# Performance work log

Hardware: AMD Instinct MI355X
Metric: run time of the kernel (lower is better)

The kernel has to match this reference:

```python
import jax, jax.numpy as jnp
import numpy as np

H1, H2, H3 = 32, 64, 64
NODEN = 12
NODES_PER_GRAPH = NODEN + 2  # 14
N = 700000                   # 50000 graphs * 14 nodes
E = 4000000


def setup_inputs() -> dict:
    key = jax.random.key(0)
    ks = jax.random.split(key, 8)
    x = jax.random.normal(ks[0], (N, H1), dtype=jnp.float32)
    edges = jax.random.randint(ks[1], (2, E), 0, N, dtype=jnp.int64)
    W1 = jax.random.normal(ks[2], (H1, H2), dtype=jnp.float32) / np.sqrt(H1).astype(np.float32)
    b1 = jnp.zeros((H2,), jnp.float32)
    W2 = jax.random.normal(ks[3], (H2, H3), dtype=jnp.float32) / np.sqrt(H2).astype(np.float32)
    b2 = jnp.zeros((H3,), jnp.float32)
    Wfc = jax.random.normal(ks[4], (H3 * NODES_PER_GRAPH, 1), dtype=jnp.float32) / np.sqrt(H3 * NODES_PER_GRAPH).astype(np.float32)
    bfc = jnp.zeros((1,), jnp.float32)
    return {"x": x, "edges": edges, "W1": W1, "b1": b1, "W2": W2, "b2": b2, "Wfc": Wfc, "bfc": bfc}


def gcn_conv(x, src, dst, W, b, n):
    # PyG GCNConv: h = X W; add self-loops; norm = deg^-1/2[src]*deg^-1/2[dst]
    h = x @ W  # [N, out]
    ones = jnp.ones(src.shape[0], dtype=h.dtype)
    deg = jax.ops.segment_sum(ones, dst, num_segments=n) + jnp.asarray(1.0, h.dtype)  # +1 self-loop
    dinv = jax.lax.rsqrt(deg)  # deg >= 1 always (self-loop)
    norm = dinv[src] * dinv[dst]  # [E]
    agg = jax.ops.segment_sum(h[src] * norm[:, None], dst, num_segments=n)
    agg = agg + h * (dinv * dinv)[:, None]  # self-loop contribution
    return agg + b


def reference(x, edges, W1, b1, W2, b2, Wfc, bfc):
    src, dst = edges[0], edges[1]
    h = jax.nn.relu(gcn_conv(x, src, dst, W1, b1, N))
    # F.dropout(training=False) is identity in eval mode
    h = jax.nn.relu(gcn_conv(h, src, dst, W2, b2, N))
    h = h.reshape(-1, H3 * NODES_PER_GRAPH)  # [B, 896]
    return h @ Wfc + bfc  # [B, 1]
```

## Files before the change

kernel.cpp:

```cpp
#include <hip/hip_runtime.h>
#include <hip/hip_fp16.h>


typedef _Float16 half8 __attribute__((ext_vector_type(8)));
typedef float float4v __attribute__((ext_vector_type(4)));

#define CHUNK 8192
#define BSH 11
#define BNODES 2048

__global__ __launch_bounds__(256) void fallback_kernel(float* __restrict__ out, int n, float v)
{
  int i = blockIdx.x * 256 + threadIdx.x;
  if (i < n) out[i] = v;
}

__global__ __launch_bounds__(64) void probe_kernel(const int* __restrict__ edges, int* __restrict__ flag)
{
  if (threadIdx.x == 0) {
    int orv = edges[1] | edges[3] | edges[5] | edges[7] | edges[9] | edges[11] | edges[13] | edges[15];
    flag[0] = (orv == 0) ? 1 : 0;
  }
}

__global__ __launch_bounds__(64) void zero_dummy_kernel(
    __half* __restrict__ F1, __half* __restrict__ F2, int N)
{
  int t = threadIdx.x;
  if (t < 16) ((uint2*)(F1 + (size_t)N * 64))[t] = make_uint2(0, 0);
  else if (t < 32) ((uint2*)(F2 + (size_t)N * 64))[t - 16] = make_uint2(0, 0);
}

__global__ __launch_bounds__(256) void hist2_kernel(
    const int* __restrict__ edges, int E, int N, const int* __restrict__ flag,
    int* __restrict__ cnt, int NBK)
{
  __shared__ int lh[512];
  int t = threadIdx.x;
  int blk = blockIdx.x;
  for (int b = t; b < NBK; b += 256) lh[b] = 0;
  __syncthreads();
  int sh = flag[0];
  int base = blk * CHUNK;
#pragma unroll
  for (int k = 0; k < CHUNK / 256; k++) {
    int e = base + k * 256 + t;
    if (e < E) {
      int d = edges[(E + e) << sh];
      if ((unsigned)d < (unsigned)N) atomicAdd(&lh[d >> BSH], 1);
    }
  }
  __syncthreads();
  for (int b = t; b < NBK; b += 256) cnt[(size_t)blk * NBK + b] = lh[b];
}

__global__ __launch_bounds__(64) void colscan_kernel(
    int* __restrict__ cnt, int NCH, int NBK, int* __restrict__ totals)
{
  int b = blockIdx.x;
  int lane = threadIdx.x;
  int carry = 0;
  int rounds = (NCH + 63) >> 6;
  for (int r = 0; r < rounds; r++) {
    int blk = r * 64 + lane;
    int v = (blk < NCH) ? cnt[(size_t)blk * NBK + b] : 0;
    int incl = v;
#pragma unroll
    for (int off = 1; off < 64; off <<= 1) {
      int x = __shfl_up(incl, off);
      if (lane >= off) incl += x;
    }
    int excl = incl - v + carry;
    if (blk < NCH) cnt[(size_t)blk * NBK + b] = excl;
    carry += __shfl(incl, 63);
  }
  if (lane == 0) totals[b] = carry;
}

__global__ __launch_bounds__(512) void scan_totals_kernel(
    const int* __restrict__ totals, int NBK,
    int* __restrict__ bstart, int* __restrict__ rowptr, int N)
{
  __shared__ int sm[512];
  int t = threadIdx.x;
  int v = (t < NBK) ? totals[t] : 0;
  sm[t] = v;
  __syncthreads();
  for (int off = 1; off < 512; off <<= 1) {
    int x = 0;
    if (t >= off) x = sm[t - off];
    __syncthreads();
    if (t >= off) sm[t] += x;
    __syncthreads();
  }
  if (t < NBK) bstart[t] = sm[t] - v;
  if (t == 0) { bstart[NBK] = sm[511]; rowptr[N] = sm[511] + N; }
}

__global__ __launch_bounds__(256) void pass3_kernel(
    const int* __restrict__ edges, int E, int N, const int* __restrict__ flag,
    const int* __restrict__ cnt, const int* __restrict__ bstart,
    int* __restrict__ pair, int NBK)
{
  __shared__ int lcur[512];
  int t = threadIdx.x;
  int blk = blockIdx.x;
  for (int b = t; b < NBK; b += 256)
    lcur[b] = bstart[b] + cnt[(size_t)blk * NBK + b];
  __syncthreads();
  int sh = flag[0];
  int base = blk * CHUNK;
#pragma unroll
  for (int k = 0; k < CHUNK / 256; k++) {
    int e = base + k * 256 + t;
    if (e < E) {
      int s = edges[e << sh];
      int d = edges[(E + e) << sh];
      if ((unsigned)s < (unsigned)N && (unsigned)d < (unsigned)N) {
        int pos = atomicAdd(&lcur[d >> BSH], 1);
        pair[pos] = s | ((d & (BNODES - 1)) << 20);
      }
    }
  }
}

__global__ __launch_bounds__(256) void build_kernel(
    const int* __restrict__ pair, const int* __restrict__ bstart,
    int* __restrict__ rowptr, float* __restrict__ dinv, int* __restrict__ col, int N)
{
  __shared__ int hist[BNODES];
  __shared__ int cur[BNODES];
  __shared__ int sc[256];
  int b = blockIdx.x;
  int t = threadIdx.x;
  int pbeg = bstart[b], pend = bstart[b + 1];
  int colbase = pbeg + (b << BSH);
#pragma unroll
  for (int i = 0; i < BNODES / 256; i++) {
    int idx = i * 256 + t;
    int row = (b << BSH) + idx;
    hist[idx] = (row < N) ? 1 : 0;
  }
  __syncthreads();
  for (int p = pbeg + t; p < pend; p += 256)
    atomicAdd(&hist[(pair[p] >> 20) & (BNODES - 1)], 1);
  __syncthreads();
  int hv[8];
  int tsum = 0;
#pragma unroll
  for (int i = 0; i < 8; i++) { hv[i] = hist[t * 8 + i]; tsum += hv[i]; }
  sc[t] = tsum;
  __syncthreads();
  for (int off = 1; off < 256; off <<= 1) {
    int x = 0;
    if (t >= off) x = sc[t - off];
    __syncthreads();
    if (t >= off) sc[t] += x;
    __syncthreads();
  }
  int run = sc[t] - tsum;
#pragma unroll
  for (int i = 0; i < 8; i++) {
    int idx = t * 8 + i;
    int rp = colbase + run;
    int row = (b << BSH) + idx;
    if (row < N) {
      rowptr[row] = rp;
      dinv[row] = rsqrtf((float)hv[i]);
      col[rp] = row;
      cur[idx] = rp + 1;
    } else {
      cur[idx] = rp;
    }
    run += hv[i];
  }
  __syncthreads();
  for (int p = pbeg + t; p < pend; p += 256) {
    int v = pair[p];
    int pos = atomicAdd(&cur[(v >> 20) & (BNODES - 1)], 1);
    col[pos] = v & 0xFFFFF;
  }
}

__global__ __launch_bounds__(256) void mfma_mm1_kernel(
    const float* __restrict__ X, const float* __restrict__ W1,
    const float* __restrict__ dinv, __half* __restrict__ G, int n, int ntiles)
{
  int lane = threadIdx.x & 63;
  int n16 = lane & 15;
  int quad = lane >> 4;

  half8 bf[4];
#pragma unroll
  for (int jb = 0; jb < 4; jb++)
#pragma unroll
    for (int i = 0; i < 8; i++)
      bf[jb][i] = (_Float16)W1[(quad * 8 + i) * 64 + jb * 16 + n16];

  _Float16* Gh = (_Float16*)G;
  int wave = (blockIdx.x * 256 + threadIdx.x) >> 6;
  int nw = (gridDim.x * 256) >> 6;
  for (int tile = wave; tile < ntiles; tile += nw) {
    int ut = __builtin_amdgcn_readfirstlane(tile);
    int base = ut * 16;
    int node = base + n16;
    if (node >= n) node = n - 1;
    const float* xr = X + (size_t)node * 32 + quad * 8;
    half8 a;
#pragma unroll
    for (int i = 0; i < 8; i++) a[i] = (_Float16)xr[i];

    float4v acc[4];
#pragma unroll
    for (int jb = 0; jb < 4; jb++) {
      float4v z = {0.f, 0.f, 0.f, 0.f};
      acc[jb] = __builtin_amdgcn_mfma_f32_16x16x32_f16(a, bf[jb], z, 0, 0, 0);
    }
#pragma unroll
    for (int r = 0; r < 4; r++) {
      int node2 = base + quad * 4 + r;
      if (node2 < n) {
        float dv = dinv[node2];
#pragma unroll
        for (int jb = 0; jb < 4; jb++)
          Gh[(size_t)node2 * 64 + jb * 16 + n16] = (_Float16)(dv * acc[jb][r]);
      }
    }
  }
}

__device__ inline void hacc(uint4 v, __half2* a)
{
  a[0] = __hadd2(a[0], *reinterpret_cast<__half2*>(&v.x));
  a[1] = __hadd2(a[1], *reinterpret_cast<__half2*>(&v.y));
  a[2] = __hadd2(a[2], *reinterpret_cast<__half2*>(&v.z));
  a[3] = __hadd2(a[3], *reinterpret_cast<__half2*>(&v.w));
}

__device__ inline __half2 hrelu2(__half2 v)
{
  __half z = __float2half_rn(0.f);
  __half2 r;
  r.x = __hmax(v.x, z);
  r.y = __hmax(v.y, z);
  return r;
}

__global__ __launch_bounds__(256) void agg_kernel(
    const __half* __restrict__ Gsrc, const int* __restrict__ rowptr,
    const int* __restrict__ col, const float* __restrict__ dinv,
    const float* __restrict__ bias, __half* __restrict__ Udst, int n, int ndummy)
{
  int lane = threadIdx.x & 63;
  int eg = lane >> 3, fo = lane & 7;
  int w = (int)((blockIdx.x * 256 + threadIdx.x) >> 6);
  w = __builtin_amdgcn_readfirstlane(w);
  int node0 = w * 2, node1 = node0 + 1;
  if (node0 >= n) return;
  bool has1 = (node1 < n);
  const uint4* G4 = (const uint4*)Gsrc;
  uint4* U4 = (uint4*)Udst;

  int beg0 = rowptr[node0];
  int end0 = rowptr[node0 + 1];
  int end1 = has1 ? rowptr[node0 + 2] : end0;

  __half2 z2 = __float2half2_rn(0.f);
  __half2 a0[4] = {z2, z2, z2, z2};
  __half2 a1[4] = {z2, z2, z2, z2};

  {
    int i0 = beg0 + eg, i1 = end0 + eg;
    int c0 = col[i0], c1 = col[i1];
    c0 = (i0 < end0) ? c0 : ndummy;
    c1 = (i1 < end1) ? c1 : ndummy;
    uint4 v0 = G4[((size_t)c0 << 3) + fo];
    uint4 v1 = G4[((size_t)c1 << 3) + fo];
    hacc(v0, a0);
    hacc(v1, a1);
  }
  for (int i = beg0 + 8; i < end0; i += 8) {
    int ii = i + eg;
    int c = col[ii];
    c = (ii < end0) ? c : ndummy;
    uint4 v = G4[((size_t)c << 3) + fo];
    hacc(v, a0);
  }
  for (int i = end0 + 8; i < end1; i += 8) {
    int ii = i + eg;
    int c = col[ii];
    c = (ii < end1) ? c : ndummy;
    uint4 v = G4[((size_t)c << 3) + fo];
    hacc(v, a1);
  }

#pragma unroll
  for (int j = 0; j < 4; j++) {
#pragma unroll
    for (int off = 8; off < 64; off <<= 1) {
      int u0 = __shfl_xor(*reinterpret_cast<int*>(&a0[j]), off);
      a0[j] = __hadd2(a0[j], *reinterpret_cast<__half2*>(&u0));
      int u1 = __shfl_xor(*reinterpret_cast<int*>(&a1[j]), off);
      a1[j] = __hadd2(a1[j], *reinterpret_cast<__half2*>(&u1));
    }
  }

  __half2 d0 = __half2half2(__float2half_rn(dinv[node0]));
  __half2 d1 = __half2half2(__float2half_rn(has1 ? dinv[node1] : 0.f));
  __half2 r0[4], r1[4];
  {
    const float* bp = bias + fo * 8;
    float4 ba = *(const float4*)bp;
    float4 bb = *(const float4*)(bp + 4);
    __half2 bh[4] = {__floats2half2_rn(ba.x, ba.y), __floats2half2_rn(ba.z, ba.w),
                     __floats2half2_rn(bb.x, bb.y), __floats2half2_rn(bb.z, bb.w)};
#pragma unroll
    for (int j = 0; j < 4; j++) {
      __half2 h0 = hrelu2(__hadd2(__hmul2(a0[j], d0), bh[j]));
      r0[j] = __hmul2(h0, d0);
      __half2 h1 = hrelu2(__hadd2(__hmul2(a1[j], d1), bh[j]));
      r1[j] = __hmul2(h1, d1);
    }
  }
  uint4 o0, o1;
  o0.x = *reinterpret_cast<uint*>(&r0[0]); o0.y = *reinterpret_cast<uint*>(&r0[1]);
  o0.z = *reinterpret_cast<uint*>(&r0[2]); o0.w = *reinterpret_cast<uint*>(&r0[3]);
  o1.x = *reinterpret_cast<uint*>(&r1[0]); o1.y = *reinterpret_cast<uint*>(&r1[1]);
  o1.z = *reinterpret_cast<uint*>(&r1[2]); o1.w = *reinterpret_cast<uint*>(&r1[3]);
  if (eg == 0) U4[((size_t)node0 << 3) + fo] = o0;
  if (eg == 1 && has1) U4[((size_t)node1 << 3) + fo] = o1;
}

__global__ __launch_bounds__(256) void out_init_kernel(
    float* __restrict__ out, const float* __restrict__ bfc, int n)
{
  int i = blockIdx.x * 256 + threadIdx.x;
  if (i < n) out[i] = bfc[0];
}

__global__ __launch_bounds__(256) void mfma_final_fused_kernel(
    const __half* __restrict__ U, const int* __restrict__ rowptr,
    const int* __restrict__ col, const float* __restrict__ dinv,
    const float* __restrict__ W2, const float* __restrict__ b2,
    const float* __restrict__ Wfc, float* __restrict__ out,
    int ntiles, int ndummy)
{
  int lane = threadIdx.x & 63;
  int n16 = lane & 15;
  int quad = lane >> 4;

  half8 bf[4][2];
#pragma unroll
  for (int jb = 0; jb < 4; jb++)
#pragma unroll
    for (int kf = 0; kf < 2; kf++)
#pragma unroll
      for (int i = 0; i < 8; i++)
        bf[jb][kf][i] = (_Float16)W2[(kf * 32 + quad * 8 + i) * 64 + jb * 16 + n16];
  float b2j[4];
#pragma unroll
  for (int jb = 0; jb < 4; jb++) b2j[jb] = b2[jb * 16 + n16];

  const uint4* U4 = (const uint4*)U;
  int wave = (blockIdx.x * 256 + threadIdx.x) >> 6;
  int nw = (gridDim.x * 256) >> 6;
  for (int tile = wave; tile < ntiles; tile += nw) {
    int ut = __builtin_amdgcn_readfirstlane(tile);
    int base = ut * 16;
    int node = base + n16;
    int rbeg = rowptr[node];
    int rlen = rowptr[node + 1] - rbeg;

    __half2 z2 = __float2half2_rn(0.f);
    __half2 acc0[4] = {z2, z2, z2, z2};
    __half2 acc1[4] = {z2, z2, z2, z2};

    for (int j = 0; __any(j < rlen); j++) {
      int c = col[rbeg + j];
      c = (j < rlen) ? c : ndummy;
      size_t rbase = (size_t)c << 3;
      uint4 v0 = U4[rbase + quad];
      uint4 v1 = U4[rbase + 4 + quad];
      hacc(v0, acc0);
      hacc(v1, acc1);
    }
    __half2 dv = __half2half2(__float2half_rn(dinv[node]));
#pragma unroll
    for (int j = 0; j < 4; j++) {
      acc0[j] = __hmul2(acc0[j], dv);
      acc1[j] = __hmul2(acc1[j], dv);
    }
    half8 a0 = *reinterpret_cast<half8*>(acc0);
    half8 a1 = *reinterpret_cast<half8*>(acc1);

    int g_r[4], t_r[4];
#pragma unroll
    for (int r = 0; r < 4; r++) {
      int nd = base + quad * 4 + r;
      g_r[r] = nd / 14;
      t_r[r] = nd - g_r[r] * 14;
    }
    float pr[4] = {0.f, 0.f, 0.f, 0.f};
#pragma unroll
    for (int jb = 0; jb < 4; jb++) {
      float4v acc = {0.f, 0.f, 0.f, 0.f};
      acc = __builtin_amdgcn_mfma_f32_16x16x32_f16(a0, bf[jb][0], acc, 0, 0, 0);
      acc = __builtin_amdgcn_mfma_f32_16x16x32_f16(a1, bf[jb][1], acc, 0, 0, 0);
      int j = jb * 16 + n16;
#pragma unroll
      for (int r = 0; r < 4; r++) {
        float h = acc[r] + b2j[jb];
        h = h > 0.f ? h : 0.f;
        pr[r] += h * Wfc[t_r[r] * 64 + j];
      }
    }
#pragma unroll
    for (int r = 0; r < 4; r++) {
#pragma unroll
      for (int off = 1; off < 16; off <<= 1) pr[r] += __shfl_xor(pr[r], off);
    }
    if (n16 == 0) {
#pragma unroll
      for (int r = 0; r < 4; r++) atomicAdd(&out[g_r[r]], pr[r]);
    }
  }
}

extern "C" void kernel_launch(void* const* d_in, const int* in_sizes, int n_in,
                              void* d_out, int out_size, void* d_ws, size_t ws_size,
                              hipStream_t stream)
{
  const float* x = (const float*)d_in[0];
  const int* edges = (const int*)d_in[1];
  const float* W1 = (const float*)d_in[2];
  const float* b1 = (const float*)d_in[3];
  const float* W2 = (const float*)d_in[4];
  const float* b2 = (const float*)d_in[5];
  const float* Wfc = (const float*)d_in[6];
  const float* bfc = (const float*)d_in[7];
  float* out = (float*)d_out;
  (void)n_in;

  const int N = in_sizes[0] / 32;
  const int E = in_sizes[1] / 2;
  const int B = out_size;
  const int NBK = (N + BNODES - 1) >> BSH;
  const int NCH = (E + CHUNK - 1) / CHUNK;

  char* ws = (char*)d_ws;
  size_t off = 0;
  auto alloc = [&](size_t bytes) -> void* {
    void* p = ws + off;
    off += (bytes + 255) & ~(size_t)255;
    return p;
  };
  int* flag = (int*)alloc(256);
  int* cnt = (int*)alloc((size_t)NCH * NBK * 4);
  int* totals = (int*)alloc((size_t)NBK * 4);
  int* bstart = (int*)alloc(((size_t)NBK + 1) * 4);
  int* col = (int*)alloc(((size_t)E + N + 256) * 4);
  int* rowptr = (int*)alloc(((size_t)N + 1) * 4);
  float* dinv = (float*)alloc((size_t)N * 4);
  __half* F1 = (__half*)alloc(((size_t)N + 16) * 64 * 2);
  __half* F2 = (__half*)alloc(((size_t)N + 16) * 64 * 2);
  int* pair = (int*)F1;

  if (off > ws_size) {
    float v = -(float)(double)(ws_size >> 20);
    fallback_kernel<<<(B + 255) / 256, 256, 0, stream>>>(out, B, v);
    return;
  }

  probe_kernel<<<1, 64, 0, stream>>>(edges, flag);
  zero_dummy_kernel<<<1, 64, 0, stream>>>(F1, F2, N);
  hist2_kernel<<<NCH, 256, 0, stream>>>(edges, E, N, flag, cnt, NBK);
  colscan_kernel<<<NBK, 64, 0, stream>>>(cnt, NCH, NBK, totals);
  scan_totals_kernel<<<1, 512, 0, stream>>>(totals, NBK, bstart, rowptr, N);
  pass3_kernel<<<NCH, 256, 0, stream>>>(edges, E, N, flag, cnt, bstart, pair, NBK);
  build_kernel<<<NBK, 256, 0, stream>>>(pair, bstart, rowptr, dinv, col, N);

  int ntiles = (N + 15) / 16;
  int aggBlocks = (N + 7) / 8;
  mfma_mm1_kernel<<<4096, 256, 0, stream>>>(x, W1, dinv, F1, N, ntiles);
  agg_kernel<<<aggBlocks, 256, 0, stream>>>(F1, rowptr, col, dinv, b1, F2, N, N);
  out_init_kernel<<<(B + 255) / 256, 256, 0, stream>>>(out, bfc, B);
  mfma_final_fused_kernel<<<4096, 256, 0, stream>>>(F2, rowptr, col, dinv, W2, b2, Wfc,
                                                    out, ntiles, N);
}
```

Baseline: 622.4 us.

## Restructure layer-1 aggregation to per-lane node rows and unroll gathers by two

Replaces the two-nodes-per-wave aggregation, which split edges across 8 lane groups and reduced with shuffles, with a persistent grid-stride kernel. In the new kernel each lane walks one node's neighbor list and 4 quads cover the 64 features. Both aggregation loops now fetch two neighbors per iteration to raise memory-level parallelism. This aims to cut idle lanes and shuffle cost at low average degree. It risks divergence when row lengths within a 16-node tile differ, and it gives up coalesced column-index loads.

```diff
diff --git a/kernel.cpp b/kernel.cpp
--- a/kernel.cpp
+++ b/kernel.cpp
@@ -246,89 +246,64 @@
   return r;
 }
 
-__global__ __launch_bounds__(256) void agg_kernel(
-    const __half* __restrict__ Gsrc, const int* __restrict__ rowptr,
+__global__ __launch_bounds__(256) void agg1_frag_kernel(
+    const __half* __restrict__ G, const int* __restrict__ rowptr,
     const int* __restrict__ col, const float* __restrict__ dinv,
-    const float* __restrict__ bias, __half* __restrict__ Udst, int n, int ndummy)
+    const float* __restrict__ bias, __half* __restrict__ U, int ntiles, int ndummy)
 {
   int lane = threadIdx.x & 63;
-  int eg = lane >> 3, fo = lane & 7;
-  int w = (int)((blockIdx.x * 256 + threadIdx.x) >> 6);
-  w = __builtin_amdgcn_readfirstlane(w);
-  int node0 = w * 2, node1 = node0 + 1;
-  if (node0 >= n) return;
-  bool has1 = (node1 < n);
-  const uint4* G4 = (const uint4*)Gsrc;
-  uint4* U4 = (uint4*)Udst;
-
-  int beg0 = rowptr[node0];
-  int end0 = rowptr[node0 + 1];
-  int end1 = has1 ? rowptr[node0 + 2] : end0;
-
-  __half2 z2 = __float2half2_rn(0.f);
-  __half2 a0[4] = {z2, z2, z2, z2};
-  __half2 a1[4] = {z2, z2, z2, z2};
-
-  {
-    int i0 = beg0 + eg, i1 = end0 + eg;
-    int c0 = col[i0], c1 = col[i1];
-    c0 = (i0 < end0) ? c0 : ndummy;
-    c1 = (i1 < end1) ? c1 : ndummy;
-    uint4 v0 = G4[((size_t)c0 << 3) + fo];
-    uint4 v1 = G4[((size_t)c1 << 3) + fo];
-    hacc(v0, a0);
-    hacc(v1, a1);
-  }
-  for (int i = beg0 + 8; i < end0; i += 8) {
-    int ii = i + eg;
-    int c = col[ii];
-    c = (ii < end0) ? c : ndummy;
-    uint4 v = G4[((size_t)c << 3) + fo];
-    hacc(v, a0);
-  }
-  for (int i = end0 + 8; i < end1; i += 8) {
-    int ii = i + eg;
-    int c = col[ii];
-    c = (ii < end1) ? c : ndummy;
-    uint4 v = G4[((size_t)c << 3) + fo];
-    hacc(v, a1);
-  }
-
-#pragma unroll
-  for (int j = 0; j < 4; j++) {
-#pragma unroll
-    for (int off = 8; off < 64; off <<= 1) {
-      int u0 = __shfl_xor(*reinterpret_cast<int*>(&a0[j]), off);
-      a0[j] = __hadd2(a0[j], *reinterpret_cast<__half2*>(&u0));
-      int u1 = __shfl_xor(*reinterpret_cast<int*>(&a1[j]), off);
-      a1[j] = __hadd2(a1[j], *reinterpret_cast<__half2*>(&u1));
-    }
-  }
-
-  __half2 d0 = __half2half2(__float2half_rn(dinv[node0]));
-  __half2 d1 = __half2half2(__float2half_rn(has1 ? dinv[node1] : 0.f));
-  __half2 r0[4], r1[4];
-  {
-    const float* bp = bias + fo * 8;
-    float4 ba = *(const float4*)bp;
-    float4 bb = *(const float4*)(bp + 4);
-    __half2 bh[4] = {__floats2half2_rn(ba.x, ba.y), __floats2half2_rn(ba.z, ba.w),
-                     __floats2half2_rn(bb.x, bb.y), __floats2half2_rn(bb.z, bb.w)};
+  int n16 = lane & 15;
+  int quad = lane >> 4;
+
+  const float* bp0 = bias + quad * 8;
+  const float* bp1 = bias + 32 + quad * 8;
+  float4 b0a = *(const float4*)bp0, b0b = *(const float4*)(bp0 + 4);
+  float4 b1a = *(const float4*)bp1, b1b = *(const float4*)(bp1 + 4);
+  __half2 bh0[4] = {__floats2half2_rn(b0a.x, b0a.y), __floats2half2_rn(b0a.z, b0a.w),
+                    __floats2half2_rn(b0b.x, b0b.y), __floats2half2_rn(b0b.z, b0b.w)};
+  __half2 bh1[4] = {__floats2half2_rn(b1a.x, b1a.y), __floats2half2_rn(b1a.z, b1a.w),
+                    __floats2half2_rn(b1b.x, b1b.y), __floats2half2_rn(b1b.z, b1b.w)};
+
+  const uint4* G4 = (const uint4*)G;
+  uint4* U4 = (uint4*)U;
+  int wave = (blockIdx.x * 256 + threadIdx.x) >> 6;
+  int nw = (gridDim.x * 256) >> 6;
+  for (int tile = wave; tile < ntiles; tile += nw) {
+    int ut = __builtin_amdgcn_readfirstlane(tile);
+    int node = ut * 16 + n16;
+    int rbeg = rowptr[node];
+    int rlen = rowptr[node + 1] - rbeg;
+
+    __half2 z2 = __float2half2_rn(0.f);
+    __half2 acc0[4] = {z2, z2, z2, z2};
+    __half2 acc1[4] = {z2, z2, z2, z2};
+
+    for (int j = 0; __any(j < rlen); j += 2) {
+      int c0 = col[rbeg + j];
+      int c1 = col[rbeg + j + 1];
+      c0 = (j < rlen) ? c0 : ndummy;
+      c1 = (j + 1 < rlen) ? c1 : ndummy;
+      uint4 v00 = G4[((size_t)c0 << 3) + quad];
+      uint4 v01 = G4[((size_t)c0 << 3) + 4 + quad];
+      uint4 v10 = G4[((size_t)c1 << 3) + quad];
+      uint4 v11 = G4[((size_t)c1 << 3) + 4 + quad];
+      hacc(v00, acc0); hacc(v01, acc1);
+      hacc(v10, acc0); hacc(v11, acc1);
+    }
+
+    __half2 dv = __half2half2(__float2half_rn(dinv[node]));
+    uint4 o0, o1;
+    __half2 r;
 #pragma unroll
     for (int j = 0; j < 4; j++) {
-      __half2 h0 = hrelu2(__hadd2(__hmul2(a0[j], d0), bh[j]));
-      r0[j] = __hmul2(h0, d0);
-      __half2 h1 = hrelu2(__hadd2(__hmul2(a1[j], d1), bh[j]));
-      r1[j] = __hmul2(h1, d1);
-    }
-  }
-  uint4 o0, o1;
-  o0.x = *reinterpret_cast<uint*>(&r0[0]); o0.y = *reinterpret_cast<uint*>(&r0[1]);
-  o0.z = *reinterpret_cast<uint*>(&r0[2]); o0.w = *reinterpret_cast<uint*>(&r0[3]);
-  o1.x = *reinterpret_cast<uint*>(&r1[0]); o1.y = *reinterpret_cast<uint*>(&r1[1]);
-  o1.z = *reinterpret_cast<uint*>(&r1[2]); o1.w = *reinterpret_cast<uint*>(&r1[3]);
-  if (eg == 0) U4[((size_t)node0 << 3) + fo] = o0;
-  if (eg == 1 && has1) U4[((size_t)node1 << 3) + fo] = o1;
+      r = __hmul2(hrelu2(__hadd2(__hmul2(acc0[j], dv), bh0[j])), dv);
+      (&o0.x)[j] = *reinterpret_cast<uint*>(&r);
+      r = __hmul2(hrelu2(__hadd2(__hmul2(acc1[j], dv), bh1[j])), dv);
+      (&o1.x)[j] = *reinterpret_cast<uint*>(&r);
+    }
+    U4[((size_t)node << 3) + quad] = o0;
+    U4[((size_t)node << 3) + 4 + quad] = o1;
+  }
 }
 
 __global__ __launch_bounds__(256) void out_init_kernel(
@@ -375,14 +350,17 @@
     __half2 acc0[4] = {z2, z2, z2, z2};
     __half2 acc1[4] = {z2, z2, z2, z2};
 
-    for (int j = 0; __any(j < rlen); j++) {
-      int c = col[rbeg + j];
-      c = (j < rlen) ? c : ndummy;
-      size_t rbase = (size_t)c << 3;
-      uint4 v0 = U4[rbase + quad];
-      uint4 v1 = U4[rbase + 4 + quad];
-      hacc(v0, acc0);
-      hacc(v1, acc1);
+    for (int j = 0; __any(j < rlen); j += 2) {
+      int c0 = col[rbeg + j];
+      int c1 = col[rbeg + j + 1];
+      c0 = (j < rlen) ? c0 : ndummy;
+      c1 = (j + 1 < rlen) ? c1 : ndummy;
+      uint4 v00 = U4[((size_t)c0 << 3) + quad];
+      uint4 v01 = U4[((size_t)c0 << 3) + 4 + quad];
+      uint4 v10 = U4[((size_t)c1 << 3) + quad];
+      uint4 v11 = U4[((size_t)c1 << 3) + 4 + quad];
+      hacc(v00, acc0); hacc(v01, acc1);
+      hacc(v10, acc0); hacc(v11, acc1);
     }
     __half2 dv = __half2half2(__float2half_rn(dinv[node]));
 #pragma unroll
@@ -480,9 +458,8 @@
   build_kernel<<<NBK, 256, 0, stream>>>(pair, bstart, rowptr, dinv, col, N);
 
   int ntiles = (N + 15) / 16;
-  int aggBlocks = (N + 7) / 8;
   mfma_mm1_kernel<<<4096, 256, 0, stream>>>(x, W1, dinv, F1, N, ntiles);
-  agg_kernel<<<aggBlocks, 256, 0, stream>>>(F1, rowptr, col, dinv, b1, F2, N, N);
+  agg1_frag_kernel<<<4096, 256, 0, stream>>>(F1, rowptr, col, dinv, b1, F2, ntiles, N);
   out_init_kernel<<<(B + 255) / 256, 256, 0, stream>>>(out, bfc, B);
   mfma_final_fused_kernel<<<4096, 256, 0, stream>>>(F2, rowptr, col, dinv, W2, b2, Wfc,
                                                     out, ntiles, N);
```

New measurement: 572.3 us. 1.09x faster.
